# Optimization experiments

Hardware: AMD Instinct MI355X
Metric: run time of the kernel (lower is better)

## Reference

```python
import jax, jax.numpy as jnp
import numpy as np

MAX_LENGTH = 41
SOS_index = 0


def setup_inputs() -> dict:
    key = jax.random.key(0)
    ks = jax.random.split(key, 16)
    B, S, H, V = 32, 41, 1024, 16384
    sc = 0.02
    inp = {
        "encoder_outputs": jax.random.normal(ks[0], (B, S, H), jnp.float32),
        "encoder_hidden": jax.random.normal(ks[1], (1, B, H), jnp.float32),
        "target_tensor": jax.random.randint(ks[2], (B, MAX_LENGTH), 0, V, jnp.int64),
        # embedding table
        "emb": jax.random.normal(ks[3], (V, H), jnp.float32) * sc,
        # Bahdanau attention params
        "Wq": jax.random.normal(ks[4], (H, H), jnp.float32) * sc,
        "bq": jnp.zeros((H,), jnp.float32),
        "Wk": jax.random.normal(ks[5], (H, H), jnp.float32) * sc,
        "bk": jnp.zeros((H,), jnp.float32),
        "Vw": jax.random.normal(ks[6], (1, H), jnp.float32) * sc,
        "bV": jnp.zeros((1,), jnp.float32),
        # LSTM params (PyTorch gate order: i, f, g, o)
        "Wih": jax.random.normal(ks[7], (4 * H, 2 * H), jnp.float32) * sc,
        "Whh": jax.random.normal(ks[8], (4 * H, H), jnp.float32) * sc,
        "bih": jnp.zeros((4 * H,), jnp.float32),
        "bhh": jnp.zeros((4 * H,), jnp.float32),
        # output projection
        "Wout": jax.random.normal(ks[9], (V, H), jnp.float32) * sc,
        "bout": jnp.zeros((V,), jnp.float32),
    }
    return inp


def reference(encoder_outputs, encoder_hidden, target_tensor, emb,
              Wq, bq, Wk, bk, Vw, bV, Wih, Whh, bih, bhh, Wout, bout):
    B = encoder_outputs.shape[0]
    H = encoder_outputs.shape[2]
    # keys projection is invariant across decode steps
    keys_proj = jnp.einsum('bsh,gh->bsg', encoder_outputs, Wk) + bk  # [B,S,H]
    # teacher-forced input tokens: SOS then target[:, :-1]
    sos = jnp.full((1, B), SOS_index, dtype=target_tensor.dtype)
    tokens = jnp.concatenate([sos, target_tensor.T[:-1]], axis=0)  # [T,B]

    h0 = encoder_hidden[0]            # [B,H]
    c0 = jnp.zeros_like(h0)

    def step(carry, tok):
        h, c = carry
        x = emb[tok]                                       # [B,H] (dropout: eval mode)
        q = h @ Wq.T + bq                                  # [B,H] query from hidden
        e = jnp.tanh(q[:, None, :] + keys_proj)            # [B,S,H]
        scores = jnp.einsum('bsh,h->bs', e, Vw[0]) + bV[0] # [B,S]
        w = jax.nn.softmax(scores, axis=-1)                # [B,S]
        ctx = jnp.einsum('bs,bsh->bh', w, encoder_outputs) # [B,H]
        xi = jnp.concatenate([x, ctx], axis=-1)            # [B,2H]
        gates = xi @ Wih.T + h @ Whh.T + (bih + bhh)       # [B,4H]
        i_g, f_g, g_g, o_g = jnp.split(gates, 4, axis=-1)
        i_g = jax.nn.sigmoid(i_g)
        f_g = jax.nn.sigmoid(f_g)
        g_g = jnp.tanh(g_g)
        o_g = jax.nn.sigmoid(o_g)
        c_new = f_g * c + i_g * g_g
        h_new = o_g * jnp.tanh(c_new)
        logits = h_new @ Wout.T + bout                     # [B,V]
        return (h_new, c_new), (logits, w)

    (h_f, c_f), (logits, attn) = jax.lax.scan(step, (h0, c0), tokens)
    decoder_outputs = jax.nn.log_softmax(logits.transpose(1, 0, 2), axis=-1)  # [B,T,V]
    attentions = attn.transpose(1, 0, 2)                                       # [B,T,S]
    return decoder_outputs, h_f[None], c_f[None], attentions
```

## Files before the change

kernel.cpp:

```cpp
#include <hip/hip_runtime.h>
#include <hip/hip_bf16.h>
#include <math.h>

#define B 32
#define S 41
#define T 41
#define H 1024
#define V 16384
#define BH (B*H)
#define NBLK 256
#define NTHR 512
#define RPB 20

typedef unsigned int uint;
typedef unsigned short ushort;
typedef __attribute__((ext_vector_type(8))) short bf16x8;
typedef __attribute__((ext_vector_type(4))) float f32x4;
typedef _Float16 h2v __attribute__((ext_vector_type(2)));

__device__ __forceinline__ float fast_sigmoid(float x){ return 1.f/(1.f + __expf(-x)); }
__device__ __forceinline__ float fast_tanh(float x){
  float e = __expf(-2.f*fabsf(x));
  float r = (1.f - e)/(1.f + e);
  return copysignf(r, x);
}
__device__ __forceinline__ ushort f2h(float f){ return __builtin_bit_cast(unsigned short, (_Float16)f); }
__device__ __forceinline__ float h2f(ushort u){ return (float)__builtin_bit_cast(_Float16, u); }
__device__ __forceinline__ h2v bc2(uint u){ return __builtin_bit_cast(h2v, u); }
__device__ __forceinline__ ushort f2bf(float f){
  uint u = __float_as_uint(f);
  u = u + 0x7FFFu + ((u>>16)&1u);
  return (ushort)(u>>16);
}

#if defined(__has_builtin)
#if __has_builtin(__builtin_amdgcn_fdot2)
#define HAS_FDOT2 1
#endif
#endif
__device__ __forceinline__ float dot2(h2v a, h2v b, float c){
#ifdef HAS_FDOT2
  return __builtin_amdgcn_fdot2(a, b, c, false);
#else
  return fmaf((float)a.x, (float)b.x, fmaf((float)a.y, (float)b.y, c));
#endif
}

__device__ __forceinline__ void st_sc_f32(float* p, float v){
  asm volatile("global_store_dword %0, %1, off sc0 sc1" :: "v"(p), "v"(v) : "memory");
}
__device__ __forceinline__ void st_sc_u32(uint* p, uint v){
  asm volatile("global_store_dword %0, %1, off sc0 sc1" :: "v"(p), "v"(v) : "memory");
}

__device__ __forceinline__ void ldx8_sc(const uint* p, uint4* r){
  asm volatile(
    "global_load_dwordx4 %0, %8, off sc0 sc1\n\t"
    "global_load_dwordx4 %1, %8, off offset:16 sc0 sc1\n\t"
    "global_load_dwordx4 %2, %8, off offset:32 sc0 sc1\n\t"
    "global_load_dwordx4 %3, %8, off offset:48 sc0 sc1\n\t"
    "global_load_dwordx4 %4, %8, off offset:64 sc0 sc1\n\t"
    "global_load_dwordx4 %5, %8, off offset:80 sc0 sc1\n\t"
    "global_load_dwordx4 %6, %8, off offset:96 sc0 sc1\n\t"
    "global_load_dwordx4 %7, %8, off offset:112 sc0 sc1\n\t"
    "s_waitcnt vmcnt(0)"
    : "=&v"(r[0]), "=&v"(r[1]), "=&v"(r[2]), "=&v"(r[3]),
      "=&v"(r[4]), "=&v"(r[5]), "=&v"(r[6]), "=&v"(r[7])
    : "v"(p) : "memory");
}
__device__ __forceinline__ void ld_qgh_sc(const float* qp, const float* gp,
                                          float4* q, float* gh){
  asm volatile(
    "global_load_dwordx4 %0, %5, off sc0 sc1\n\t"
    "global_load_dwordx4 %1, %5, off offset:16 sc0 sc1\n\t"
    "global_load_dwordx4 %2, %5, off offset:32 sc0 sc1\n\t"
    "global_load_dwordx4 %3, %5, off offset:48 sc0 sc1\n\t"
    "global_load_dword  %4, %6, off sc0 sc1\n\t"
    "s_waitcnt vmcnt(0)"
    : "=&v"(q[0]), "=&v"(q[1]), "=&v"(q[2]), "=&v"(q[3]), "=&v"(*gh)
    : "v"(qp), "v"(gp) : "memory");
}

__device__ __forceinline__ void gbar_full(uint* bar, int phase){
  asm volatile("s_waitcnt vmcnt(0)" ::: "memory");
  __syncthreads();
  if (threadIdx.x == 0){
    const int gid = blockIdx.x >> 5;
    __builtin_amdgcn_fence(__ATOMIC_RELEASE, "agent");
    uint old = __hip_atomic_fetch_add(&bar[gid*32], 1u, __ATOMIC_RELAXED, __HIP_MEMORY_SCOPE_AGENT);
    if ((old & 31u) == 31u){
      uint r = __hip_atomic_fetch_add(&bar[256], 1u, __ATOMIC_RELAXED, __HIP_MEMORY_SCOPE_AGENT);
      if ((r & 7u) == 7u){
        #pragma unroll
        for (int g = 0; g < 8; ++g)
          __hip_atomic_store(&bar[288+g*32], (uint)phase, __ATOMIC_RELAXED, __HIP_MEMORY_SCOPE_AGENT);
      }
    }
    while (__hip_atomic_load(&bar[288+gid*32], __ATOMIC_RELAXED, __HIP_MEMORY_SCOPE_AGENT) < (uint)phase)
      __builtin_amdgcn_s_sleep(2);
  }
  __syncthreads();
}

__device__ __forceinline__ void gbar_x(uint* bar, int phase,
                                       uint my_xcd, uint my_cnt, uint nx, uint lb){
  asm volatile("s_waitcnt vmcnt(0)" ::: "memory");
  __syncthreads();
  if (threadIdx.x == 0){
    uint old = __hip_atomic_fetch_add(&bar[512 + my_xcd*16], 1u, __ATOMIC_RELAXED, __HIP_MEMORY_SCOPE_AGENT);
    if (old == lb*my_cnt + (my_cnt - 1u)){
      uint r = __hip_atomic_fetch_add(&bar[640], 1u, __ATOMIC_RELAXED, __HIP_MEMORY_SCOPE_AGENT);
      if (r == lb*nx + (nx - 1u)){
        #pragma unroll
        for (int g = 0; g < 8; ++g)
          __hip_atomic_store(&bar[704+g*16], (uint)phase, __ATOMIC_RELAXED, __HIP_MEMORY_SCOPE_AGENT);
      }
    }
    while (__hip_atomic_load(&bar[704+my_xcd*16], __ATOMIC_RELAXED, __HIP_MEMORY_SCOPE_AGENT) < (uint)phase)
      __builtin_amdgcn_s_sleep(1);
  }
  __syncthreads();
}

__global__ __launch_bounds__(256) void k_init(const float* __restrict__ eh,
                                              ushort* __restrict__ h16, uint* __restrict__ bar){
  int i = blockIdx.x*256 + threadIdx.x;
  h16[i] = f2h(eh[i]);
  if (i < 1024) bar[i] = 0;
}

__global__ __launch_bounds__(256) void k_bsum(const float* __restrict__ a,
                                              const float* __restrict__ b, float* __restrict__ o){
  int i = blockIdx.x*256 + threadIdx.x;
  o[i] = a[i] + b[i];
}

__global__ __launch_bounds__(256) void k_gather(const float* __restrict__ emb,
    const int* __restrict__ tgt, float* __restrict__ Xall){
  int r = blockIdx.x;
  int t = r / B, b = r % B;
  int tok = (t==0) ? 0 : tgt[b*T + (t-1)];
  const float4* src = (const float4*)(emb + (size_t)tok*H);
  float4* dst = (float4*)(Xall + (size_t)r*H);
  dst[threadIdx.x] = src[threadIdx.x];
}

__global__ __launch_bounds__(256) void k_cvt16(const float* __restrict__ src,
                                               ushort* __restrict__ dst, int n8){
  int i = blockIdx.x*256 + threadIdx.x;
  if (i >= n8) return;
  const float4* s4 = (const float4*)src + (size_t)i*2;
  float4 a = s4[0], b = s4[1];
  union { ushort us[8]; uint4 v; } p;
  p.us[0]=f2h(a.x); p.us[1]=f2h(a.y); p.us[2]=f2h(a.z); p.us[3]=f2h(a.w);
  p.us[4]=f2h(b.x); p.us[5]=f2h(b.y); p.us[6]=f2h(b.z); p.us[7]=f2h(b.w);
  ((uint4*)dst)[i] = p.v;
}

__global__ __launch_bounds__(256) void k_bgemm(const float* __restrict__ A,
    const float* __restrict__ W, const float* __restrict__ bias, float* __restrict__ C,
    int M, int N, int wstride, int woff)
{
  __shared__ ushort As[128*40];
  __shared__ ushort Bs[128*40];
  const int tid = threadIdx.x;
  const int n0 = blockIdx.x*128, m0 = blockIdx.y*128;
  const int row = tid>>1, half = tid&1;
  const int lane = tid & 63, widx = tid >> 6;
  const int wm = (widx>>1)*64, wn = (widx&1)*64;

  int arow = m0 + row; if (arow > M-1) arow = M-1;
  const float* ga = A + (size_t)arow*1024 + half*16;
  const float* gw = W + (size_t)(n0+row)*wstride + woff + half*16;
  ushort* sa = &As[row*40 + half*16];
  ushort* sb = &Bs[row*40 + half*16];

  f32x4 acc[4][4] = {};

  for (int k0 = 0; k0 < 1024; k0 += 32) {
    float4 a0 = *(const float4*)(ga+k0),   a1 = *(const float4*)(ga+k0+4);
    float4 a2 = *(const float4*)(ga+k0+8), a3 = *(const float4*)(ga+k0+12);
    float4 w0 = *(const float4*)(gw+k0),   w1 = *(const float4*)(gw+k0+4);
    float4 w2 = *(const float4*)(gw+k0+8), w3 = *(const float4*)(gw+k0+12);
    __syncthreads();
    {
      union { ushort us[8]; uint4 v; } p, q;
      p.us[0]=f2bf(a0.x); p.us[1]=f2bf(a0.y); p.us[2]=f2bf(a0.z); p.us[3]=f2bf(a0.w);
      p.us[4]=f2bf(a1.x); p.us[5]=f2bf(a1.y); p.us[6]=f2bf(a1.z); p.us[7]=f2bf(a1.w);
      q.us[0]=f2bf(a2.x); q.us[1]=f2bf(a2.y); q.us[2]=f2bf(a2.z); q.us[3]=f2bf(a2.w);
      q.us[4]=f2bf(a3.x); q.us[5]=f2bf(a3.y); q.us[6]=f2bf(a3.z); q.us[7]=f2bf(a3.w);
      *(uint4*)sa = p.v; *(uint4*)(sa+8) = q.v;
      p.us[0]=f2bf(w0.x); p.us[1]=f2bf(w0.y); p.us[2]=f2bf(w0.z); p.us[3]=f2bf(w0.w);
      p.us[4]=f2bf(w1.x); p.us[5]=f2bf(w1.y); p.us[6]=f2bf(w1.z); p.us[7]=f2bf(w1.w);
      q.us[0]=f2bf(w2.x); q.us[1]=f2bf(w2.y); q.us[2]=f2bf(w2.z); q.us[3]=f2bf(w2.w);
      q.us[4]=f2bf(w3.x); q.us[5]=f2bf(w3.y); q.us[6]=f2bf(w3.z); q.us[7]=f2bf(w3.w);
      *(uint4*)sb = p.v; *(uint4*)(sb+8) = q.v;
    }
    __syncthreads();
    bf16x8 af[4], bf[4];
    #pragma unroll
    for (int i=0;i<4;i++)
      af[i] = *(const bf16x8*)&As[(wm + i*16 + (lane&15))*40 + (lane>>4)*8];
    #pragma unroll
    for (int j=0;j<4;j++)
      bf[j] = *(const bf16x8*)&Bs[(wn + j*16 + (lane&15))*40 + (lane>>4)*8];
    #pragma unroll
    for (int i=0;i<4;i++)
      #pragma unroll
      for (int j=0;j<4;j++)
        acc[i][j] = __builtin_amdgcn_mfma_f32_16x16x32_bf16(af[i], bf[j], acc[i][j], 0, 0, 0);
  }

  #pragma unroll
  for (int i=0;i<4;i++){
    #pragma unroll
    for (int j=0;j<4;j++){
      int n = n0 + wn + j*16 + (lane&15);
      float bv = bias ? bias[n] : 0.f;
      #pragma unroll
      for (int qq=0;qq<4;qq++){
        int m = m0 + wm + i*16 + ((lane>>4)<<2) + qq;
        if (m < M) C[(size_t)m*N + n] = acc[i][j][qq] + bv;
      }
    }
  }
}

__global__ __launch_bounds__(512, 2) void k_loop(
    const ushort* __restrict__ Wc16,
    const float* __restrict__ bq,
    const ushort* __restrict__ keys16,
    const float* __restrict__ Vw, const float* __restrict__ bV,
    const float* __restrict__ GxF,
    const ushort* __restrict__ encW16,
    float* __restrict__ qg,
    float* __restrict__ ghg,
    ushort* __restrict__ h16,
    float* __restrict__ hhist,
    float* __restrict__ attn_out,
    float* __restrict__ hf, float* __restrict__ cf,
    uint* __restrict__ bar)
{
  __shared__ __align__(16) uint   w_lds[RPB*516];
  __shared__ __align__(16) ushort ew_lds[512*42];
  __shared__ __align__(16) float  red[RPB*512];
  __shared__ float sc_sh[64];
  __shared__ float ga[512];
  __shared__ float hsh[128];

  const int tid = threadIdx.x;
  const int bid = blockIdx.x;
  const int pb_b = bid >> 3, pb_mc = bid & 7;
  const int lane = tid & 63, wv = tid >> 6;
  uint* h16u = (uint*)h16;

  const int pa_b = tid & 31, pa_ks = tid >> 5;
  const int gn = (tid >> 7)*H + pb_mc*128 + (tid & 127);

  const int na = bid*RPB + (tid>>5);
  const int nb = bid*RPB + 16 + (tid>>5);
  const float bqa = (na < H) ? bq[na] : 0.f;
  const float bqb = (tid < 128 && nb < H) ? bq[nb] : 0.f;

  uint my_xcd = 0, my_cnt = 0, nx = 8, lb = 0;
  if (tid == 0){
    uint x;
    asm volatile("s_getreg_b32 %0, hwreg(20, 0, 32)" : "=s"(x));
    my_xcd = x & 7u;
    __hip_atomic_fetch_add(&bar[832 + my_xcd*16], 1u, __ATOMIC_RELAXED, __HIP_MEMORY_SCOPE_AGENT);
  }

  for (int i = tid; i < RPB*128; i += NTHR){
    int r = i >> 7, j = i & 127;
    uint4 v = *((const uint4*)(Wc16 + (size_t)(bid*RPB + r)*1024) + j);
    *(uint4*)&w_lds[r*516 + j*4] = v;
  }
  for (int s = 0; s < S; ++s)
    ew_lds[tid*42 + s] = encW16[((size_t)pb_b*S + s)*4096 + gn];
  float vreg[16];
  {
    const float4* vp = (const float4*)(Vw + lane*16);
    *(float4*)&vreg[0] = vp[0]; *(float4*)&vreg[4]  = vp[1];
    *(float4*)&vreg[8] = vp[2]; *(float4*)&vreg[12] = vp[3];
  }
  const float bV0 = bV[0];
  float creg = 0.f;
  __syncthreads();

  for (int t = 0; t < T; ++t) {
    float gxv;
    {
      uint4 hr[8];
      ldx8_sc((const uint*)h16u + pa_b*512 + pa_ks*32, hr);
      float part[RPB];
      #pragma unroll
      for (int r = 0; r < RPB; ++r){
        const uint* wr = &w_lds[r*516 + pa_ks*32];
        float a0 = 0.f, a1 = 0.f;
        #pragma unroll
        for (int j = 0; j < 8; ++j){
          uint4 w = *(const uint4*)(wr + j*4);
          uint4 h = hr[j];
          a0 = dot2(bc2(w.x), bc2(h.x), a0);
          a1 = dot2(bc2(w.y), bc2(h.y), a1);
          a0 = dot2(bc2(w.z), bc2(h.z), a0);
          a1 = dot2(bc2(w.w), bc2(h.w), a1);
        }
        part[r] = a0 + a1;
      }
      #pragma unroll
      for (int r = 0; r < RPB; ++r) red[r*512 + pa_ks*32 + pa_b] = part[r];
      __syncthreads();
      {
        int r = tid >> 5, b2 = tid & 31;
        const float* rp = &red[r*512 + b2];
        float s = 0.f;
        #pragma unroll
        for (int k2 = 0; k2 < 16; ++k2) s += rp[k2*32];
        if (na < H) st_sc_f32(&qg[b2*H + na], s + bqa);
        else        st_sc_f32(&ghg[(size_t)b2*4*H + (na - H)], s);
      }
      if (tid < 128){
        int r = 16 + (tid >> 5), b2 = tid & 31;
        const float* rp = &red[r*512 + b2];
        float s = 0.f;
        #pragma unroll
        for (int k2 = 0; k2 < 16; ++k2) s += rp[k2*32];
        if (nb < H) st_sc_f32(&qg[b2*H + nb], s + bqb);
        else        st_sc_f32(&ghg[(size_t)b2*4*H + (nb - H)], s);
      }
      gxv = GxF[((size_t)t*B + pb_b)*4*H + gn];
    }
    if (t == 0){
      gbar_full(bar, 1);
      if (tid == 0){
        my_cnt = __hip_atomic_load(&bar[832 + my_xcd*16], __ATOMIC_RELAXED, __HIP_MEMORY_SCOPE_AGENT);
        uint n = 0;
        #pragma unroll
        for (int g = 0; g < 8; ++g)
          n += (__hip_atomic_load(&bar[832 + g*16], __ATOMIC_RELAXED, __HIP_MEMORY_SCOPE_AGENT) != 0u) ? 1u : 0u;
        nx = n;
      }
    } else {
      gbar_x(bar, 2*t + 1, my_xcd, my_cnt, nx, lb); lb++;
    }

    {
      float4 q4[4]; float ghv;
      ld_qgh_sc(qg + pb_b*H + lane*16, ghg + (size_t)pb_b*4*H + gn, q4, &ghv);
      float qarr[16];
      *(float4*)&qarr[0] = q4[0]; *(float4*)&qarr[4]  = q4[1];
      *(float4*)&qarr[8] = q4[2]; *(float4*)&qarr[12] = q4[3];

      for (int s = wv; s < S; s += 8) {
        const ushort* kr = keys16 + ((size_t)pb_b*S + s)*H + lane*16;
        uint4 k0 = *(const uint4*)kr;
        uint4 k1 = *(const uint4*)(kr + 8);
        float part = 0.f;
        #define SC2(u, e) { h2v hh = bc2(u); \
          part += fast_tanh(qarr[e]   + (float)hh.x) * vreg[e]; \
          part += fast_tanh(qarr[e+1] + (float)hh.y) * vreg[e+1]; }
        SC2(k0.x,0) SC2(k0.y,2) SC2(k0.z,4) SC2(k0.w,6)
        SC2(k1.x,8) SC2(k1.y,10) SC2(k1.z,12) SC2(k1.w,14)
        #undef SC2
        #pragma unroll
        for (int off = 32; off > 0; off >>= 1) part += __shfl_xor(part, off);
        if (lane == 0) sc_sh[s] = part + bV0;
      }
      __syncthreads();
      if (tid < 64) {
        float val = (tid < S) ? sc_sh[tid] : -1e30f;
        float m = val;
        #pragma unroll
        for (int off = 32; off > 0; off >>= 1) m = fmaxf(m, __shfl_xor(m, off));
        float e = (tid < S) ? __expf(val - m) : 0.f;
        float ssum = e;
        #pragma unroll
        for (int off = 32; off > 0; off >>= 1) ssum += __shfl_xor(ssum, off);
        if (tid < S) {
          float w = e / ssum;
          sc_sh[tid] = w;
          if (pb_mc == 0) attn_out[((size_t)pb_b*T + t)*S + tid] = w;
        }
      }
      __syncthreads();
      {
        float acc = gxv + ghv;
        const ushort* ep = &ew_lds[tid*42];
        #pragma unroll
        for (int s = 0; s < S; ++s)
          acc = fmaf(sc_sh[s], h2f(ep[s]), acc);
        ga[tid] = acc;
      }
      __syncthreads();
      if (tid < 128) {
        float ig = fast_sigmoid(ga[tid]);
        float fg = fast_sigmoid(ga[128+tid]);
        float gg = fast_tanh   (ga[256+tid]);
        float og = fast_sigmoid(ga[384+tid]);
        creg = fg*creg + ig*gg;
        float hn = og * fast_tanh(creg);
        int m = pb_mc*128 + tid;
        hsh[tid] = hn;
        __builtin_nontemporal_store(hn, &hhist[((size_t)pb_b*T + t)*H + m]);
        if (t == T-1) { hf[pb_b*H + m] = hn; cf[pb_b*H + m] = creg; }
      }
      __syncthreads();
      if (tid < 64) {
        uint pk = (uint)f2h(hsh[2*tid]) | ((uint)f2h(hsh[2*tid+1]) << 16);
        st_sc_u32(&h16u[(size_t)pb_b*512 + pb_mc*64 + tid], pk);
      }
    }
    if (t < T-1) { gbar_x(bar, 2*t + 2, my_xcd, my_cnt, nx, lb); lb++; }
  }
}

__global__ __launch_bounds__(256) void k_logsm(float* __restrict__ p_all)
{
  float* p = p_all + (size_t)blockIdx.x * V;
  const int tid = threadIdx.x;
  const int lane = tid & 63, wave = tid >> 6;
  __shared__ float red[4];
  float4 v[16];
  float m = -1e30f;
  #pragma unroll
  for (int j=0;j<16;j++){
    v[j] = *(const float4*)(p + 4*(tid + 256*j));
    m = fmaxf(m, fmaxf(fmaxf(v[j].x, v[j].y), fmaxf(v[j].z, v[j].w)));
  }
  #pragma unroll
  for (int off=32; off>0; off>>=1) m = fmaxf(m, __shfl_xor(m, off));
  if (lane==0) red[wave] = m;
  __syncthreads();
  m = fmaxf(fmaxf(red[0], red[1]), fmaxf(red[2], red[3]));
  float ssum = 0.f;
  #pragma unroll
  for (int j=0;j<16;j++){
    ssum += __expf(v[j].x - m) + __expf(v[j].y - m) + __expf(v[j].z - m) + __expf(v[j].w - m);
  }
  #pragma unroll
  for (int off=32; off>0; off>>=1) ssum += __shfl_xor(ssum, off);
  __syncthreads();
  if (lane==0) red[wave] = ssum;
  __syncthreads();
  float lse = m + __logf(red[0] + red[1] + red[2] + red[3]);
  #pragma unroll
  for (int j=0;j<16;j++){
    float4 o; o.x = v[j].x - lse; o.y = v[j].y - lse; o.z = v[j].z - lse; o.w = v[j].w - lse;
    *(float4*)(p + 4*(tid + 256*j)) = o;
  }
}

extern "C" void kernel_launch(void* const* d_in, const int* in_sizes, int n_in,
                              void* d_out, int out_size, void* d_ws, size_t ws_size,
                              hipStream_t stream) {
  const float* enc   = (const float*)d_in[0];
  const float* ehid  = (const float*)d_in[1];
  const int*   tgt   = (const int*)  d_in[2];
  const float* emb   = (const float*)d_in[3];
  const float* Wq    = (const float*)d_in[4];
  const float* bq    = (const float*)d_in[5];
  const float* Wk    = (const float*)d_in[6];
  const float* bk    = (const float*)d_in[7];
  const float* Vw    = (const float*)d_in[8];
  const float* bV    = (const float*)d_in[9];
  const float* Wih   = (const float*)d_in[10];
  const float* Whh   = (const float*)d_in[11];
  const float* bih   = (const float*)d_in[12];
  const float* bhh   = (const float*)d_in[13];
  const float* Wout  = (const float*)d_in[14];
  const float* bout  = (const float*)d_in[15];

  float* out  = (float*)d_out;
  float* dec  = out;
  float* hf   = out + (size_t)B*T*V;
  float* cf   = hf + BH;
  float* attn = cf + BH;

  float*  Xall   = dec;
  float*  keysF  = dec +  1343488;
  float*  GxF    = dec +  2686976;
  float*  encWF  = dec +  8060928;
  ushort* keys16 = (ushort*)(dec + 13434880);
  ushort* encW16 = (ushort*)(dec + 14106624);
  ushort* Wc16   = (ushort*)(dec + 16793600);

  float* ws = (float*)d_ws;
  float*  hhist = ws;
  float*  bsum  = ws + 1343488;
  ushort* h16   = (ushort*)(ws + 1347584);
  float*  qg    = ws + 1363968;
  float*  ghg   = ws + 1396736;
  uint*   bar   = (uint*)(ws + 1527808);

  k_init<<<BH/256, 256, 0, stream>>>(ehid, h16, bar);
  k_bsum<<<(4*H)/256, 256, 0, stream>>>(bih, bhh, bsum);
  k_gather<<<T*B, 256, 0, stream>>>(emb, tgt, Xall);

  { dim3 g(H/128, 11);     k_bgemm<<<g, 256, 0, stream>>>(enc,  Wk,  bk,     keysF, B*S, H,   H,   0); }
  { dim3 g((4*H)/128, 11); k_bgemm<<<g, 256, 0, stream>>>(Xall, Wih, bsum,   GxF,   T*B, 4*H, 2*H, 0); }
  { dim3 g((4*H)/128, 11); k_bgemm<<<g, 256, 0, stream>>>(enc,  Wih, nullptr,encWF, B*S, 4*H, 2*H, H); }

  k_cvt16<<<(B*S*H/8 + 255)/256, 256, 0, stream>>>(keysF, keys16, B*S*H/8);
  k_cvt16<<<(B*S*4*H/8 + 255)/256, 256, 0, stream>>>(encWF, encW16, B*S*4*H/8);
  k_cvt16<<<(H*H/8 + 255)/256, 256, 0, stream>>>(Wq,  Wc16,             H*H/8);
  k_cvt16<<<(4*H*H/8 + 255)/256, 256, 0, stream>>>(Whh, Wc16 + (size_t)H*H, 4*H*H/8);

  {
    void* kargs[] = {
      (void*)&Wc16, (void*)&bq, (void*)&keys16, (void*)&Vw, (void*)&bV,
      (void*)&GxF, (void*)&encW16, (void*)&qg, (void*)&ghg,
      (void*)&h16, (void*)&hhist, (void*)&attn, (void*)&hf, (void*)&cf, (void*)&bar
    };
    hipLaunchCooperativeKernel((const void*)k_loop, dim3(NBLK), dim3(NTHR), kargs, 0, stream);
  }

  { dim3 g(V/128, 11);     k_bgemm<<<g, 256, 0, stream>>>(hhist, Wout, bout, dec, B*T, V, H, 0); }
  k_logsm<<<B*T, 256, 0, stream>>>(dec);
}
```

Before: 1.299 ms.

## Split attention scores across batch-group blocks and flatten grid barriers

Replaces the hierarchical XCD-aware grid barriers with a single flat atomic counter per phase. It also distributes the attention score computation across the 8 blocks that share a batch row: each wave computes one sequence position and publishes it to global memory, and a per-batch 8-block barrier follows before the softmax. This removes redundant score work per block, at the cost of an extra small barrier each step and 256-way contention on a single counter.

```diff
diff --git a/kernel.cpp b/kernel.cpp
--- a/kernel.cpp
+++ b/kernel.cpp
@@ -53,6 +53,12 @@
   asm volatile("global_store_dword %0, %1, off sc0 sc1" :: "v"(p), "v"(v) : "memory");
 }
 
+__device__ __forceinline__ float ld_sc_f32(const float* p){
+  float r;
+  asm volatile("global_load_dword %0, %1, off sc0 sc1\n\ts_waitcnt vmcnt(0)"
+               : "=v"(r) : "v"(p) : "memory");
+  return r;
+}
 __device__ __forceinline__ void ldx8_sc(const uint* p, uint4* r){
   asm volatile(
     "global_load_dwordx4 %0, %8, off sc0 sc1\n\t"
@@ -81,42 +87,12 @@
     : "v"(qp), "v"(gp) : "memory");
 }
 
-__device__ __forceinline__ void gbar_full(uint* bar, int phase){
+__device__ __forceinline__ void gbar_flat(uint* cnt, uint target){
   asm volatile("s_waitcnt vmcnt(0)" ::: "memory");
   __syncthreads();
   if (threadIdx.x == 0){
-    const int gid = blockIdx.x >> 5;
-    __builtin_amdgcn_fence(__ATOMIC_RELEASE, "agent");
-    uint old = __hip_atomic_fetch_add(&bar[gid*32], 1u, __ATOMIC_RELAXED, __HIP_MEMORY_SCOPE_AGENT);
-    if ((old & 31u) == 31u){
-      uint r = __hip_atomic_fetch_add(&bar[256], 1u, __ATOMIC_RELAXED, __HIP_MEMORY_SCOPE_AGENT);
-      if ((r & 7u) == 7u){
-        #pragma unroll
-        for (int g = 0; g < 8; ++g)
-          __hip_atomic_store(&bar[288+g*32], (uint)phase, __ATOMIC_RELAXED, __HIP_MEMORY_SCOPE_AGENT);
-      }
-    }
-    while (__hip_atomic_load(&bar[288+gid*32], __ATOMIC_RELAXED, __HIP_MEMORY_SCOPE_AGENT) < (uint)phase)
-      __builtin_amdgcn_s_sleep(2);
-  }
-  __syncthreads();
-}
-
-__device__ __forceinline__ void gbar_x(uint* bar, int phase,
-                                       uint my_xcd, uint my_cnt, uint nx, uint lb){
-  asm volatile("s_waitcnt vmcnt(0)" ::: "memory");
-  __syncthreads();
-  if (threadIdx.x == 0){
-    uint old = __hip_atomic_fetch_add(&bar[512 + my_xcd*16], 1u, __ATOMIC_RELAXED, __HIP_MEMORY_SCOPE_AGENT);
-    if (old == lb*my_cnt + (my_cnt - 1u)){
-      uint r = __hip_atomic_fetch_add(&bar[640], 1u, __ATOMIC_RELAXED, __HIP_MEMORY_SCOPE_AGENT);
-      if (r == lb*nx + (nx - 1u)){
-        #pragma unroll
-        for (int g = 0; g < 8; ++g)
-          __hip_atomic_store(&bar[704+g*16], (uint)phase, __ATOMIC_RELAXED, __HIP_MEMORY_SCOPE_AGENT);
-      }
-    }
-    while (__hip_atomic_load(&bar[704+my_xcd*16], __ATOMIC_RELAXED, __HIP_MEMORY_SCOPE_AGENT) < (uint)phase)
+    __hip_atomic_fetch_add(cnt, 1u, __ATOMIC_RELAXED, __HIP_MEMORY_SCOPE_AGENT);
+    while (__hip_atomic_load(cnt, __ATOMIC_RELAXED, __HIP_MEMORY_SCOPE_AGENT) < target)
       __builtin_amdgcn_s_sleep(1);
   }
   __syncthreads();
@@ -239,7 +215,8 @@
     float* __restrict__ hhist,
     float* __restrict__ attn_out,
     float* __restrict__ hf, float* __restrict__ cf,
-    uint* __restrict__ bar)
+    uint* __restrict__ bar,
+    float* __restrict__ pscore)
 {
   __shared__ __align__(16) uint   w_lds[RPB*516];
   __shared__ __align__(16) ushort ew_lds[512*42];
@@ -262,13 +239,10 @@
   const float bqa = (na < H) ? bq[na] : 0.f;
   const float bqb = (tid < 128 && nb < H) ? bq[nb] : 0.f;
 
-  uint my_xcd = 0, my_cnt = 0, nx = 8, lb = 0;
-  if (tid == 0){
-    uint x;
-    asm volatile("s_getreg_b32 %0, hwreg(20, 0, 32)" : "=s"(x));
-    my_xcd = x & 7u;
-    __hip_atomic_fetch_add(&bar[832 + my_xcd*16], 1u, __ATOMIC_RELAXED, __HIP_MEMORY_SCOPE_AGENT);
-  }
+  uint* qcnt = &bar[0];
+  uint* hcnt = &bar[16];
+  uint* scnt = &bar[256 + pb_b*8];
+  const int my_s = pb_mc + 8*wv;
 
   for (int i = tid; i < RPB*128; i += NTHR){
     int r = i >> 7, j = i & 127;
@@ -331,19 +305,7 @@
       }
       gxv = GxF[((size_t)t*B + pb_b)*4*H + gn];
     }
-    if (t == 0){
-      gbar_full(bar, 1);
-      if (tid == 0){
-        my_cnt = __hip_atomic_load(&bar[832 + my_xcd*16], __ATOMIC_RELAXED, __HIP_MEMORY_SCOPE_AGENT);
-        uint n = 0;
-        #pragma unroll
-        for (int g = 0; g < 8; ++g)
-          n += (__hip_atomic_load(&bar[832 + g*16], __ATOMIC_RELAXED, __HIP_MEMORY_SCOPE_AGENT) != 0u) ? 1u : 0u;
-        nx = n;
-      }
-    } else {
-      gbar_x(bar, 2*t + 1, my_xcd, my_cnt, nx, lb); lb++;
-    }
+    gbar_flat(qcnt, 256u*(uint)(t+1));
 
     {
       float4 q4[4]; float ghv;
@@ -352,8 +314,8 @@
       *(float4*)&qarr[0] = q4[0]; *(float4*)&qarr[4]  = q4[1];
       *(float4*)&qarr[8] = q4[2]; *(float4*)&qarr[12] = q4[3];
 
-      for (int s = wv; s < S; s += 8) {
-        const ushort* kr = keys16 + ((size_t)pb_b*S + s)*H + lane*16;
+      if (my_s < S) {
+        const ushort* kr = keys16 + ((size_t)pb_b*S + my_s)*H + lane*16;
         uint4 k0 = *(const uint4*)kr;
         uint4 k1 = *(const uint4*)(kr + 8);
         float part = 0.f;
@@ -365,11 +327,18 @@
         #undef SC2
         #pragma unroll
         for (int off = 32; off > 0; off >>= 1) part += __shfl_xor(part, off);
-        if (lane == 0) sc_sh[s] = part + bV0;
+        if (lane == 0) st_sc_f32(&pscore[pb_b*64 + my_s], part + bV0);
+      }
+      asm volatile("s_waitcnt vmcnt(0)" ::: "memory");
+      __syncthreads();
+      if (tid == 0){
+        __hip_atomic_fetch_add(scnt, 1u, __ATOMIC_RELAXED, __HIP_MEMORY_SCOPE_AGENT);
+        while (__hip_atomic_load(scnt, __ATOMIC_RELAXED, __HIP_MEMORY_SCOPE_AGENT) < 8u*(uint)(t+1))
+          __builtin_amdgcn_s_sleep(1);
       }
       __syncthreads();
       if (tid < 64) {
-        float val = (tid < S) ? sc_sh[tid] : -1e30f;
+        float val = (tid < S) ? ld_sc_f32(&pscore[pb_b*64 + tid]) : -1e30f;
         float m = val;
         #pragma unroll
         for (int off = 32; off > 0; off >>= 1) m = fmaxf(m, __shfl_xor(m, off));
@@ -411,7 +380,7 @@
         st_sc_u32(&h16u[(size_t)pb_b*512 + pb_mc*64 + tid], pk);
       }
     }
-    if (t < T-1) { gbar_x(bar, 2*t + 2, my_xcd, my_cnt, nx, lb); lb++; }
+    if (t < T-1) gbar_flat(hcnt, 256u*(uint)(t+1));
   }
 }
 
@@ -492,6 +461,7 @@
   float*  qg    = ws + 1363968;
   float*  ghg   = ws + 1396736;
   uint*   bar   = (uint*)(ws + 1527808);
+  float*  pscore= ws + 1528832;
 
   k_init<<<BH/256, 256, 0, stream>>>(ehid, h16, bar);
   k_bsum<<<(4*H)/256, 256, 0, stream>>>(bih, bhh, bsum);
@@ -510,7 +480,8 @@
     void* kargs[] = {
       (void*)&Wc16, (void*)&bq, (void*)&keys16, (void*)&Vw, (void*)&bV,
       (void*)&GxF, (void*)&encW16, (void*)&qg, (void*)&ghg,
-      (void*)&h16, (void*)&hhist, (void*)&attn, (void*)&hf, (void*)&cf, (void*)&bar
+      (void*)&h16, (void*)&hhist, (void*)&attn, (void*)&hf, (void*)&cf,
+      (void*)&bar, (void*)&pscore
     };
     hipLaunchCooperativeKernel((const void*)k_loop, dim3(NBLK), dim3(NTHR), kargs, 0, stream);
   }
```

Measured after the change: 1.568 ms. 1.21x slower.
